# Optimization experiments

Hardware: AMD Instinct MI355X
Metric: run time of the kernel (lower is better)

## Reference

```python
import jax, jax.numpy as jnp
import numpy as np

B, N, M, D, KV, H = 4, 1024, 1024, 1024, 1024, 16
HD = D // H


def setup_inputs() -> dict:
    key = jax.random.key(0)
    ks = jax.random.split(key, 9)
    s = 0.02
    return {
        "query": jax.random.normal(ks[0], (B, N, D), jnp.float32),
        "key_value": jax.random.normal(ks[1], (B, M, KV), jnp.float32),
        "mask": jax.random.bernoulli(ks[2], 0.1, (B, M)),  # True = masked out
        "Wq": jax.random.normal(ks[3], (D, D), jnp.float32) * s,
        "bq": jnp.zeros((D,), jnp.float32),
        "Wkv": jax.random.normal(ks[4], (KV, 2 * D), jnp.float32) * s,
        "bkv": jnp.zeros((2 * D,), jnp.float32),
        "Wp": jax.random.normal(ks[5], (D, 2), jnp.float32) * s,
        "bp": jnp.zeros((2,), jnp.float32),
    }


def reference(query, key_value, mask, Wq, bq, Wkv, bkv, Wp, bp):
    b, n, d = query.shape
    m = key_value.shape[1]
    scale = HD ** (-0.5)
    # projections
    queries = (query @ Wq + bq).reshape(b, n, H, HD)
    kv = (key_value @ Wkv + bkv).reshape(b, m, 2, H, HD)
    keys, values = kv[:, :, 0], kv[:, :, 1]
    # scores in bnmh layout (as the original einsum)
    attention = jnp.einsum('bnhd,bmhd->bnmh', queries, keys) * scale
    # mask [b,m] -> unsqueeze(1) -> [b,1,m] -> unsqueeze(3) -> [b,1,m,1]
    attention = jnp.where(mask[:, None, :, None], -jnp.inf, attention)
    attention = jax.nn.softmax(attention, axis=2)
    outputs = jnp.einsum('bnmh,bmhd->bnhd', attention, values).reshape(b, n, d)
    outputs = outputs @ Wp + bp
    return outputs, attention
```

## Files before the change

### kernel.cpp

```cpp
#include <hip/hip_runtime.h>

typedef unsigned short u16;
typedef unsigned int u32;
typedef __bf16 bf16x8 __attribute__((ext_vector_type(8)));
typedef float f32x4 __attribute__((ext_vector_type(4)));

#define MFMA16 __builtin_amdgcn_mfma_f32_16x16x32_bf16


__device__ __forceinline__ float b2f(u16 u){ u32 x = ((u32)u)<<16; float f; __builtin_memcpy(&f,&x,4); return f; }
__device__ __forceinline__ u16 f2b(float f){ u32 x; __builtin_memcpy(&x,&f,4); return (u16)((x + 0x7fffu + ((x>>16)&1u)) >> 16); }
__device__ __forceinline__ bf16x8 ldf(const u16* p){ uint4 v = *(const uint4*)p; return __builtin_bit_cast(bf16x8, v); }
__device__ __forceinline__ u32 pk(u16 a, u16 b){ return (u32)a | ((u32)b<<16); }

__device__ __forceinline__ void stage16(const u16* g, u16* l) {
  __builtin_amdgcn_global_load_lds(
      (const __attribute__((address_space(1))) void*)g,
      (__attribute__((address_space(3))) void*)l, 16, 0, 0);
}

__device__ __forceinline__ uint4 ld8(const void* base, size_t off, int f32) {
  if (f32) {
    const float* p = (const float*)base + off;
    f32x4 a = *(const f32x4*)p;
    f32x4 b = *(const f32x4*)(p + 4);
    uint4 r;
    r.x = pk(f2b(a[0]), f2b(a[1]));
    r.y = pk(f2b(a[2]), f2b(a[3]));
    r.z = pk(f2b(b[0]), f2b(b[1]));
    r.w = pk(f2b(b[2]), f2b(b[3]));
    return r;
  }
  return *(const uint4*)((const u16*)base + off);
}
__device__ __forceinline__ float lds1(const void* base, size_t off, int f32) {
  return f32 ? ((const float*)base)[off] : b2f(((const u16*)base)[off]);
}

__global__ __launch_bounds__(256) void detect_dtype(const u32* __restrict__ q, int* __restrict__ flag) {
  __shared__ int cnt;
  if (threadIdx.x == 0) cnt = 0;
  __syncthreads();
  int c = 0;
#pragma unroll
  for (int i = 0; i < 4; i++) {
    u32 w = q[threadIdx.x + i*256];
    u32 e = (w >> 7) & 0xFFu;
    c += (e >= 100u && e <= 140u) ? 1 : 0;
  }
#pragma unroll
  for (int m = 1; m <= 32; m <<= 1) c += __shfl_xor(c, m);
  if ((threadIdx.x & 63) == 0) atomicAdd(&cnt, c);
  __syncthreads();
  if (threadIdx.x == 0) flag[0] = (cnt < 512) ? 1 : 0;
}

__global__ __launch_bounds__(1024) void mask_convert(const void* __restrict__ mraw,
                                                     float* __restrict__ maskF) {
  __shared__ u32 orv;
  const int t = threadIdx.x;
  if (t == 0) orv = 0u;
  __syncthreads();
  u32 o = ((const u32*)mraw)[t];
#pragma unroll
  for (int m = 1; m <= 32; m <<= 1) o |= __shfl_xor(o, m);
  if ((t & 63) == 0) atomicOr(&orv, o);
  __syncthreads();
  const u32 orall = orv;
  int mode;
  if ((orall & ~0x01010101u) == 0u) mode = (orall <= 1u) ? 0 : 1;
  else if (orall & 0x0000FF80u)     mode = 2;
  else                              mode = 3;
  const float NEGINF = -__builtin_inff();
#pragma unroll
  for (int i = t; i < 4096; i += 1024) {
    bool mm;
    if      (mode == 0) mm = ((const int*)mraw)[i] != 0;
    else if (mode == 1) mm = ((const unsigned char*)mraw)[i] != 0;
    else if (mode == 2) mm = ((const u16*)mraw)[i] != 0;
    else                mm = ((const float*)mraw)[i] != 0.f;
    maskF[i] = mm ? NEGINF : 0.f;
  }
}

__global__ __launch_bounds__(256) void to_bf16(const void* __restrict__ in, const int* __restrict__ flag,
                                               u16* __restrict__ out) {
  const int f32 = flag[0];
  const size_t idx = ((size_t)blockIdx.x*256 + threadIdx.x)*8;
  *(uint4*)(out + idx) = ld8(in, idx, f32);
}

__global__ __launch_bounds__(256) void transpose_w(const void* __restrict__ in, const int* __restrict__ flag,
                                                   u16* __restrict__ out, int R, int C) {
  __shared__ u16 tile[64][72];
  const int f32 = flag[0];
  const int t = threadIdx.x;
  const int c0 = blockIdx.x*64, r0 = blockIdx.y*64;
  const int lr = t >> 2, cs = (t & 3)*16;
#pragma unroll
  for (int i=0;i<2;i++)
    *(uint4*)&tile[lr][cs + i*8] = ld8(in, (size_t)(r0 + lr)*C + c0 + cs + i*8, f32);
  __syncthreads();
  const int c = t >> 2, rs = (t & 3)*16;
  u16 v[16];
#pragma unroll
  for (int j=0;j<16;j++) v[j] = tile[rs + j][c];
  uint4 u0 = { pk(v[0],v[1]), pk(v[2],v[3]), pk(v[4],v[5]), pk(v[6],v[7]) };
  uint4 u1 = { pk(v[8],v[9]), pk(v[10],v[11]), pk(v[12],v[13]), pk(v[14],v[15]) };
  u16* op = out + (size_t)(c0 + c)*R + r0 + rs;
  *(uint4*)op = u0;
  *(uint4*)(op + 8) = u1;
}

__global__ __launch_bounds__(256) void gemm_nt(const u16* __restrict__ A, const u16* __restrict__ Bt,
                                               const void* __restrict__ bias, const int* __restrict__ flag,
                                               u16* __restrict__ C, int Mdim, int Ndim, int Kdim) {
  __shared__ u16 As[128][64];
  __shared__ u16 Bs[128][64];
  const int f32 = flag[0];
  const int tid = threadIdx.x, l = tid & 63, w = tid >> 6;
  const int n0 = blockIdx.x * 128, m0 = blockIdx.y * 128;
  const int wr = (w & 1) * 64, wc = (w >> 1) * 64;
  const int lr = l & 15, lg = l >> 4;
  f32x4 acc[4][4];
#pragma unroll
  for (int i=0;i<4;i++)
#pragma unroll
    for (int j=0;j<4;j++) acc[i][j] = (f32x4){0.f,0.f,0.f,0.f};
  const int srow = l >> 3;
  const int scol = (l & 7) * 8;
  const u16* Ab = A  + (size_t)m0 * Kdim;
  const u16* Bb = Bt + (size_t)n0 * Kdim;
  for (int k0 = 0; k0 < Kdim; k0 += 64) {
    __syncthreads();
#pragma unroll
    for (int i = 0; i < 4; i++) {
      const int seg = i*4 + w;
      stage16(Ab + (size_t)(seg*8 + srow)*Kdim + k0 + scol, &As[seg*8][0]);
      stage16(Bb + (size_t)(seg*8 + srow)*Kdim + k0 + scol, &Bs[seg*8][0]);
    }
    __syncthreads();
    bf16x8 af[4][2], bfr[4][2];
#pragma unroll
    for (int rt=0; rt<4; rt++) {
      af[rt][0] = ldf(&As[wr + rt*16 + lr][lg*8]);
      af[rt][1] = ldf(&As[wr + rt*16 + lr][32 + lg*8]);
    }
#pragma unroll
    for (int ct=0; ct<4; ct++) {
      bfr[ct][0] = ldf(&Bs[wc + ct*16 + lr][lg*8]);
      bfr[ct][1] = ldf(&Bs[wc + ct*16 + lr][32 + lg*8]);
    }
#pragma unroll
    for (int rt=0; rt<4; rt++)
#pragma unroll
      for (int ct=0; ct<4; ct++) {
        acc[rt][ct] = MFMA16(af[rt][0], bfr[ct][0], acc[rt][ct], 0,0,0);
        acc[rt][ct] = MFMA16(af[rt][1], bfr[ct][1], acc[rt][ct], 0,0,0);
      }
  }
#pragma unroll
  for (int ct=0; ct<4; ct++) {
    const int col = n0 + wc + ct*16 + lr;
    const float bv = lds1(bias, col, f32);
#pragma unroll
    for (int rt=0; rt<4; rt++)
#pragma unroll
      for (int r=0; r<4; r++) {
        const int row = m0 + wr + rt*16 + lg*4 + r;
        C[(size_t)row * Ndim + col] = f2b(acc[rt][ct][r] + bv);
      }
  }
}

__global__ __launch_bounds__(256) void build_vt(const u16* __restrict__ KVb, u16* __restrict__ Vt) {
  __shared__ u16 tile[64][72];
  const int t = threadIdx.x;
  const int m0 = blockIdx.x*64, h = blockIdx.y, b = blockIdx.z;
  const int mr = t >> 2, cs = (t & 3)*16;
  const u16* src = KVb + (size_t)(b*1024 + m0 + mr)*2048 + 1024 + h*64;
#pragma unroll
  for (int i=0;i<2;i++)
    *(uint4*)&tile[mr][cs + i*8] = *(const uint4*)(src + cs + i*8);
  __syncthreads();
  const int hd = t >> 2, ms = (t & 3)*16;
  u16 v[16];
#pragma unroll
  for (int j=0;j<16;j++) v[j] = tile[ms + j][hd];
  uint4 u0 = { pk(v[0],v[1]), pk(v[2],v[3]), pk(v[4],v[5]), pk(v[6],v[7]) };
  uint4 u1 = { pk(v[8],v[9]), pk(v[10],v[11]), pk(v[12],v[13]), pk(v[14],v[15]) };
  u16* op = Vt + (size_t)((b*16 + h)*64 + hd)*1024 + m0 + ms;
  *(uint4*)op = u0;
  *(uint4*)(op + 8) = u1;
}

__global__ __launch_bounds__(256) void attn_kern(const u16* __restrict__ Qb, const u16* __restrict__ KVb,
                                                 const u16* __restrict__ Vt, const float* __restrict__ maskF,
                                                 u16* __restrict__ Pbuf, u16* __restrict__ Obuf) {
  __shared__ u16 Ks[128][72];
  __shared__ u16 Vts[64][136];
  __shared__ u16 Ps[4][16][136];
  __shared__ float mlds[128];
  const int tid = threadIdx.x, l = tid & 63, w = tid >> 6;
  const int lr = l & 15, lg = l >> 4;
  const int n0 = blockIdx.x * 64, h = blockIdx.y, b = blockIdx.z;
  const float NEGINF = -__builtin_inff();
  const float scale2 = 0.125f * 1.44269504088896f;

  bf16x8 qf[2];
  {
    const u16* Qsrc = Qb + (size_t)(b*1024 + n0 + 16*w + lr)*1024 + h*64 + lg*8;
    qf[0] = ldf(Qsrc);
    qf[1] = ldf(Qsrc + 32);
  }
  float mrow[4] = {NEGINF,NEGINF,NEGINF,NEGINF};
  float lrow[4] = {0.f,0.f,0.f,0.f};

  const int ksr = tid >> 1, kss = (tid & 1)*32;
  const u16* Kbase = KVb + (size_t)(b*1024)*2048 + h*64;
  const u16* Vbase = Vt + (size_t)((b*16 + h)*64)*1024;
  const int vsr = tid >> 2, vss = (tid & 3)*32;

  for (int c = 0; c < 8; c++) {
    const int m0 = c * 128;
    __syncthreads();
#pragma unroll
    for (int i=0;i<4;i++)
      *(uint4*)&Ks[ksr][kss + i*8] = *(const uint4*)(Kbase + (size_t)(m0 + ksr)*2048 + kss + i*8);
    if (tid < 128) mlds[tid] = maskF[b*1024 + m0 + tid];
    __syncthreads();
    f32x4 sa[8];
#pragma unroll
    for (int ct=0; ct<8; ct++) {
      sa[ct] = (f32x4){0.f,0.f,0.f,0.f};
      bf16x8 k0 = ldf(&Ks[ct*16 + lr][lg*8]);
      bf16x8 k1 = ldf(&Ks[ct*16 + lr][32 + lg*8]);
      sa[ct] = MFMA16(qf[0], k0, sa[ct], 0,0,0);
      sa[ct] = MFMA16(qf[1], k1, sa[ct], 0,0,0);
    }
    float cmax[4] = {NEGINF,NEGINF,NEGINF,NEGINF};
#pragma unroll
    for (int ct=0; ct<8; ct++) {
      const float mv = mlds[ct*16 + lr];
#pragma unroll
      for (int r=0;r<4;r++) {
        float s = fmaf(sa[ct][r], scale2, mv);
        sa[ct][r] = s;
        cmax[r] = fmaxf(cmax[r], s);
      }
    }
#pragma unroll
    for (int r=0;r<4;r++) {
#pragma unroll
      for (int m = 1; m <= 8; m <<= 1) cmax[r] = fmaxf(cmax[r], __shfl_xor(cmax[r], m));
      const float mnew = fmaxf(mrow[r], cmax[r]);
      float se = 0.f;
#pragma unroll
      for (int ct=0; ct<8; ct++) se += exp2f(fmaxf(sa[ct][r] - mnew, -1000.f));
#pragma unroll
      for (int m = 1; m <= 8; m <<= 1) se += __shfl_xor(se, m);
      lrow[r] = lrow[r] * exp2f(fmaxf(mrow[r] - mnew, -1000.f)) + se;
      mrow[r] = mnew;
    }
  }
  float rinv[4];
#pragma unroll
  for (int r=0;r<4;r++) rinv[r] = (lrow[r] > 0.f) ? 1.f / lrow[r] : 0.f;

  f32x4 oacc[4];
#pragma unroll
  for (int vt=0; vt<4; vt++) oacc[vt] = (f32x4){0.f,0.f,0.f,0.f};
  for (int c = 0; c < 8; c++) {
    const int m0 = c*128;
    __syncthreads();
#pragma unroll
    for (int i=0;i<4;i++)
      *(uint4*)&Ks[ksr][kss + i*8] = *(const uint4*)(Kbase + (size_t)(m0 + ksr)*2048 + kss + i*8);
#pragma unroll
    for (int i=0;i<4;i++)
      *(uint4*)&Vts[vsr][vss + i*8] = *(const uint4*)(Vbase + (size_t)vsr*1024 + m0 + vss + i*8);
    if (tid < 128) mlds[tid] = maskF[b*1024 + m0 + tid];
    __syncthreads();
    f32x4 sa[8];
#pragma unroll
    for (int ct=0; ct<8; ct++) {
      sa[ct] = (f32x4){0.f,0.f,0.f,0.f};
      bf16x8 k0 = ldf(&Ks[ct*16 + lr][lg*8]);
      bf16x8 k1 = ldf(&Ks[ct*16 + lr][32 + lg*8]);
      sa[ct] = MFMA16(qf[0], k0, sa[ct], 0,0,0);
      sa[ct] = MFMA16(qf[1], k1, sa[ct], 0,0,0);
    }
#pragma unroll
    for (int ct=0; ct<8; ct++) {
      const float mv = mlds[ct*16 + lr];
#pragma unroll
      for (int r=0;r<4;r++) {
        float ex = fmaxf(fmaf(sa[ct][r], scale2, mv) - mrow[r], -1000.f);
        float p = exp2f(ex) * rinv[r];
        Ps[w][lg*4 + r][ct*16 + lr] = f2b(p);
      }
    }
    {
      const int pr = l >> 2, psg = (l & 3) * 32;
      u16* gp = Pbuf + (size_t)((b*16 + h)*1024 + n0 + 16*w + pr)*1024 + m0 + psg;
#pragma unroll
      for (int i=0;i<4;i++)
        *(uint4*)(gp + i*8) = *(const uint4*)&Ps[w][pr][psg + i*8];
    }
    bf16x8 pa[4];
#pragma unroll
    for (int t=0;t<4;t++) pa[t] = ldf(&Ps[w][lr][t*32 + lg*8]);
#pragma unroll
    for (int vt=0; vt<4; vt++) {
#pragma unroll
      for (int t=0;t<4;t++) {
        bf16x8 bv = ldf(&Vts[vt*16 + lr][t*32 + lg*8]);
        oacc[vt] = MFMA16(pa[t], bv, oacc[vt], 0,0,0);
      }
    }
  }
#pragma unroll
  for (int vt=0; vt<4; vt++)
#pragma unroll
    for (int r=0;r<4;r++) {
      const int row = b*1024 + n0 + 16*w + lg*4 + r;
      const int col = h*64 + vt*16 + lr;
      Obuf[(size_t)row*1024 + col] = f2b(oacc[vt][r]);
    }
}

__global__ __launch_bounds__(256) void transpose_p(const u16* __restrict__ Pbuf, float* __restrict__ out) {
  __shared__ u16 t2[16][1024];
  const int t = threadIdx.x;
  const int n = blockIdx.x, b = blockIdx.y;
  const int h = t >> 4, sg = (t & 15)*64;
  const u16* src = Pbuf + (size_t)((b*16 + h)*1024 + n)*1024 + sg;
#pragma unroll
  for (int i=0;i<8;i++)
    *(uint4*)&t2[h][sg + i*8] = *(const uint4*)(src + i*8);
  __syncthreads();
  float* dst = out + (size_t)(b*1024 + n)*16384;
#pragma unroll
  for (int mi=0; mi<4; mi++) {
    const int m = t + mi*256;
#pragma unroll
    for (int q=0; q<4; q++) {
      f32x4 v;
#pragma unroll
      for (int j=0; j<4; j++) v[j] = b2f(t2[q*4 + j][m]);
      *(f32x4*)(dst + (size_t)m*16 + q*4) = v;
    }
  }
}

__global__ __launch_bounds__(256) void proj_out_k(const u16* __restrict__ Obuf, const void* __restrict__ Wp,
                                                  const void* __restrict__ bp, const int* __restrict__ flag,
                                                  float* __restrict__ out0) {
  const int f32 = flag[0];
  const int l = threadIdx.x & 63, w = threadIdx.x >> 6;
  const int row = blockIdx.x*4 + w;
  const u16* op = Obuf + (size_t)row*1024 + l*16;
  float d0 = 0.f, d1 = 0.f;
#pragma unroll
  for (int j=0;j<16;j++) {
    const float o = b2f(op[j]);
    d0 = fmaf(o, lds1(Wp, (size_t)(l*16 + j)*2,     f32), d0);
    d1 = fmaf(o, lds1(Wp, (size_t)(l*16 + j)*2 + 1, f32), d1);
  }
#pragma unroll
  for (int m=1; m<=32; m<<=1) { d0 += __shfl_xor(d0, m); d1 += __shfl_xor(d1, m); }
  if (l == 0) {
    out0[row*2]   = d0 + lds1(bp, 0, f32);
    out0[row*2+1] = d1 + lds1(bp, 1, f32);
  }
}

extern "C" void kernel_launch(void* const* d_in, const int* in_sizes, int n_in,
                              void* d_out, int out_size, void* d_ws, size_t ws_size,
                              hipStream_t stream) {
  const void* query     = d_in[0];
  const void* key_value = d_in[1];
  const void* mask      = d_in[2];
  const void* Wq        = d_in[3];
  const void* bq        = d_in[4];
  const void* Wkv       = d_in[5];
  const void* bkv       = d_in[6];
  const void* Wp        = d_in[7];
  const void* bp        = d_in[8];
  float* out0     = (float*)d_out;
  float* attn_out = (float*)d_out + 8192;

  char* ws = (char*)d_ws;
  u16*   WqT   = (u16*)(ws);
  u16*   WkvT  = (u16*)(ws + (2u<<20));
  u16*   Qb    = (u16*)(ws + (6u<<20));
  u16*   KVb   = (u16*)(ws + (14u<<20));
  u16*   Vt    = (u16*)(ws + (30u<<20));
  u16*   Obuf  = (u16*)(ws + (38u<<20));
  float* maskF = (float*)(ws + (46u<<20));
  int*   flag  = (int*)(ws + (46u<<20) + 16384);
  u16*   Pbuf  = (u16*)(ws + (47u<<20));
  u16*   Qc    = (u16*)(ws + (47u<<20));
  u16*   KVc   = (u16*)(ws + (55u<<20));

  detect_dtype<<<1, 256, 0, stream>>>((const u32*)query, flag);
  mask_convert<<<1, 1024, 0, stream>>>(mask, maskF);
  to_bf16<<<2048, 256, 0, stream>>>(query,     flag, Qc);
  to_bf16<<<2048, 256, 0, stream>>>(key_value, flag, KVc);
  transpose_w<<<dim3(16,16), 256, 0, stream>>>(Wq, flag, WqT, 1024, 1024);
  transpose_w<<<dim3(32,16), 256, 0, stream>>>(Wkv, flag, WkvT, 1024, 2048);
  gemm_nt<<<dim3(8,32),  256, 0, stream>>>(Qc,  WqT,  bq,  flag, Qb,  4096, 1024, 1024);
  gemm_nt<<<dim3(16,32), 256, 0, stream>>>(KVc, WkvT, bkv, flag, KVb, 4096, 2048, 1024);
  build_vt<<<dim3(16,16,4), 256, 0, stream>>>(KVb, Vt);
  attn_kern<<<dim3(16,16,4), 256, 0, stream>>>(Qb, KVb, Vt, maskF, Pbuf, Obuf);
  transpose_p<<<dim3(1024,4), 256, 0, stream>>>(Pbuf, attn_out);
  proj_out_k<<<dim3(1024), 256, 0, stream>>>(Obuf, Wp, bp, flag, out0);
}
```

Before: 574.3 us.

## Fuse two-pass attention into single online-softmax pass with deferred probability rescaling

The attention kernel previously ran QK^T twice: one pass for the row max and sum, and a second to form normalized probabilities and multiply by V. It now runs a single online-softmax pass that rescales the output accumulator per chunk. It stores unnormalized probabilities together with per-chunk running maxima and the final max and inverse sum. The transpose kernel then applies the correction factor exp2(m_chunk - m_final) * rinv while writing the fp32 attention output. This removes the duplicated K loads and MFMA work, at the cost of extra small scratch buffers, a per-element LUT multiply in the transpose, and bf16 rounding of the unnormalized values before scaling.

```diff
diff --git a/kernel.cpp b/kernel.cpp
--- a/kernel.cpp
+++ b/kernel.cpp
@@ -196,7 +196,8 @@
 
 __global__ __launch_bounds__(256) void attn_kern(const u16* __restrict__ Qb, const u16* __restrict__ KVb,
                                                  const u16* __restrict__ Vt, const float* __restrict__ maskF,
-                                                 u16* __restrict__ Pbuf, u16* __restrict__ Obuf) {
+                                                 u16* __restrict__ Pbuf, u16* __restrict__ Obuf,
+                                                 float* __restrict__ Sc, float* __restrict__ Fin) {
   __shared__ u16 Ks[128][72];
   __shared__ u16 Vts[64][136];
   __shared__ u16 Ps[4][16][136];
@@ -215,6 +216,9 @@
   }
   float mrow[4] = {NEGINF,NEGINF,NEGINF,NEGINF};
   float lrow[4] = {0.f,0.f,0.f,0.f};
+  f32x4 oacc[4];
+#pragma unroll
+  for (int vt=0; vt<4; vt++) oacc[vt] = (f32x4){0.f,0.f,0.f,0.f};
 
   const int ksr = tid >> 1, kss = (tid & 1)*32;
   const u16* Kbase = KVb + (size_t)(b*1024)*2048 + h*64;
@@ -222,11 +226,14 @@
   const int vsr = tid >> 2, vss = (tid & 3)*32;
 
   for (int c = 0; c < 8; c++) {
-    const int m0 = c * 128;
+    const int m0 = c*128;
     __syncthreads();
 #pragma unroll
     for (int i=0;i<4;i++)
       *(uint4*)&Ks[ksr][kss + i*8] = *(const uint4*)(Kbase + (size_t)(m0 + ksr)*2048 + kss + i*8);
+#pragma unroll
+    for (int i=0;i<4;i++)
+      *(uint4*)&Vts[vsr][vss + i*8] = *(const uint4*)(Vbase + (size_t)vsr*1024 + m0 + vss + i*8);
     if (tid < 128) mlds[tid] = maskF[b*1024 + m0 + tid];
     __syncthreads();
     f32x4 sa[8];
@@ -249,57 +256,32 @@
         cmax[r] = fmaxf(cmax[r], s);
       }
     }
+    float al[4];
 #pragma unroll
     for (int r=0;r<4;r++) {
 #pragma unroll
       for (int m = 1; m <= 8; m <<= 1) cmax[r] = fmaxf(cmax[r], __shfl_xor(cmax[r], m));
       const float mnew = fmaxf(mrow[r], cmax[r]);
+      al[r] = exp2f(fmaxf(mrow[r] - mnew, -1000.f));
       float se = 0.f;
 #pragma unroll
-      for (int ct=0; ct<8; ct++) se += exp2f(fmaxf(sa[ct][r] - mnew, -1000.f));
+      for (int ct=0; ct<8; ct++) {
+        float p = exp2f(fmaxf(sa[ct][r] - mnew, -1000.f));
+        sa[ct][r] = p;
+        se += p;
+      }
 #pragma unroll
       for (int m = 1; m <= 8; m <<= 1) se += __shfl_xor(se, m);
-      lrow[r] = lrow[r] * exp2f(fmaxf(mrow[r] - mnew, -1000.f)) + se;
+      lrow[r] = lrow[r] * al[r] + se;
       mrow[r] = mnew;
-    }
-  }
-  float rinv[4];
-#pragma unroll
-  for (int r=0;r<4;r++) rinv[r] = (lrow[r] > 0.f) ? 1.f / lrow[r] : 0.f;
-
-  f32x4 oacc[4];
-#pragma unroll
-  for (int vt=0; vt<4; vt++) oacc[vt] = (f32x4){0.f,0.f,0.f,0.f};
-  for (int c = 0; c < 8; c++) {
-    const int m0 = c*128;
-    __syncthreads();
-#pragma unroll
-    for (int i=0;i<4;i++)
-      *(uint4*)&Ks[ksr][kss + i*8] = *(const uint4*)(Kbase + (size_t)(m0 + ksr)*2048 + kss + i*8);
-#pragma unroll
-    for (int i=0;i<4;i++)
-      *(uint4*)&Vts[vsr][vss + i*8] = *(const uint4*)(Vbase + (size_t)vsr*1024 + m0 + vss + i*8);
-    if (tid < 128) mlds[tid] = maskF[b*1024 + m0 + tid];
-    __syncthreads();
-    f32x4 sa[8];
-#pragma unroll
-    for (int ct=0; ct<8; ct++) {
-      sa[ct] = (f32x4){0.f,0.f,0.f,0.f};
-      bf16x8 k0 = ldf(&Ks[ct*16 + lr][lg*8]);
-      bf16x8 k1 = ldf(&Ks[ct*16 + lr][32 + lg*8]);
-      sa[ct] = MFMA16(qf[0], k0, sa[ct], 0,0,0);
-      sa[ct] = MFMA16(qf[1], k1, sa[ct], 0,0,0);
-    }
-#pragma unroll
-    for (int ct=0; ct<8; ct++) {
-      const float mv = mlds[ct*16 + lr];
-#pragma unroll
-      for (int r=0;r<4;r++) {
-        float ex = fmaxf(fmaf(sa[ct][r], scale2, mv) - mrow[r], -1000.f);
-        float p = exp2f(ex) * rinv[r];
-        Ps[w][lg*4 + r][ct*16 + lr] = f2b(p);
-      }
-    }
+      if (lr == 0)
+        Sc[(((size_t)b*1024 + n0 + 16*w + lg*4 + r)*16 + h)*8 + c] = mnew;
+    }
+#pragma unroll
+    for (int ct=0; ct<8; ct++)
+#pragma unroll
+      for (int r=0;r<4;r++)
+        Ps[w][lg*4 + r][ct*16 + lr] = f2b(sa[ct][r]);
     {
       const int pr = l >> 2, psg = (l & 3) * 32;
       u16* gp = Pbuf + (size_t)((b*16 + h)*1024 + n0 + 16*w + pr)*1024 + m0 + psg;
@@ -307,6 +289,10 @@
       for (int i=0;i<4;i++)
         *(uint4*)(gp + i*8) = *(const uint4*)&Ps[w][pr][psg + i*8];
     }
+#pragma unroll
+    for (int vt=0; vt<4; vt++)
+#pragma unroll
+      for (int r=0;r<4;r++) oacc[vt][r] *= al[r];
     bf16x8 pa[4];
 #pragma unroll
     for (int t=0;t<4;t++) pa[t] = ldf(&Ps[w][lr][t*32 + lg*8]);
@@ -319,18 +305,33 @@
       }
     }
   }
+  float rinv[4];
+#pragma unroll
+  for (int r=0;r<4;r++) rinv[r] = (lrow[r] > 0.f) ? 1.f / lrow[r] : 0.f;
 #pragma unroll
   for (int vt=0; vt<4; vt++)
 #pragma unroll
     for (int r=0;r<4;r++) {
       const int row = b*1024 + n0 + 16*w + lg*4 + r;
       const int col = h*64 + vt*16 + lr;
-      Obuf[(size_t)row*1024 + col] = f2b(oacc[vt][r]);
-    }
-}
-
-__global__ __launch_bounds__(256) void transpose_p(const u16* __restrict__ Pbuf, float* __restrict__ out) {
+      Obuf[(size_t)row*1024 + col] = f2b(oacc[vt][r] * rinv[r]);
+    }
+  if (lr == 0) {
+#pragma unroll
+    for (int r=0;r<4;r++) {
+      const size_t fo = (((size_t)b*1024 + n0 + 16*w + lg*4 + r)*16 + h)*2;
+      Fin[fo]   = mrow[r];
+      Fin[fo+1] = rinv[r];
+    }
+  }
+}
+
+__global__ __launch_bounds__(256) void transpose_p(const u16* __restrict__ Pbuf,
+                                                   const float* __restrict__ Sc,
+                                                   const float* __restrict__ Fin,
+                                                   float* __restrict__ out) {
   __shared__ u16 t2[16][1024];
+  __shared__ float slut[128];
   const int t = threadIdx.x;
   const int n = blockIdx.x, b = blockIdx.y;
   const int h = t >> 4, sg = (t & 15)*64;
@@ -338,16 +339,25 @@
 #pragma unroll
   for (int i=0;i<8;i++)
     *(uint4*)&t2[h][sg + i*8] = *(const uint4*)(src + i*8);
+  if (t < 128) {
+    const int hh = t >> 3, cc = t & 7;
+    const size_t base = ((size_t)b*1024 + n)*16 + hh;
+    const float mc = Sc[base*8 + cc];
+    const float mf = Fin[base*2];
+    const float ri = Fin[base*2 + 1];
+    slut[t] = exp2f(fmaxf(mc - mf, -1000.f)) * ri;
+  }
   __syncthreads();
   float* dst = out + (size_t)(b*1024 + n)*16384;
 #pragma unroll
   for (int mi=0; mi<4; mi++) {
     const int m = t + mi*256;
+    const int c = m >> 7;
 #pragma unroll
     for (int q=0; q<4; q++) {
       f32x4 v;
 #pragma unroll
-      for (int j=0; j<4; j++) v[j] = b2f(t2[q*4 + j][m]);
+      for (int j=0; j<4; j++) v[j] = b2f(t2[q*4 + j][m]) * slut[(q*4 + j)*8 + c];
       *(f32x4*)(dst + (size_t)m*16 + q*4) = v;
     }
   }
@@ -400,6 +410,8 @@
   float* maskF = (float*)(ws + (46u<<20));
   int*   flag  = (int*)(ws + (46u<<20) + 16384);
   u16*   Pbuf  = (u16*)(ws + (47u<<20));
+  float* Sc    = (float*)(ws + (175u<<20));
+  float* Fin   = (float*)(ws + (177u<<20));
   u16*   Qc    = (u16*)(ws + (47u<<20));
   u16*   KVc   = (u16*)(ws + (55u<<20));
 
@@ -412,7 +424,7 @@
   gemm_nt<<<dim3(8,32),  256, 0, stream>>>(Qc,  WqT,  bq,  flag, Qb,  4096, 1024, 1024);
   gemm_nt<<<dim3(16,32), 256, 0, stream>>>(KVc, WkvT, bkv, flag, KVb, 4096, 2048, 1024);
   build_vt<<<dim3(16,16,4), 256, 0, stream>>>(KVb, Vt);
-  attn_kern<<<dim3(16,16,4), 256, 0, stream>>>(Qb, KVb, Vt, maskF, Pbuf, Obuf);
-  transpose_p<<<dim3(1024,4), 256, 0, stream>>>(Pbuf, attn_out);
+  attn_kern<<<dim3(16,16,4), 256, 0, stream>>>(Qb, KVb, Vt, maskF, Pbuf, Obuf, Sc, Fin);
+  transpose_p<<<dim3(1024,4), 256, 0, stream>>>(Pbuf, Sc, Fin, attn_out);
   proj_out_k<<<dim3(1024), 256, 0, stream>>>(Obuf, Wp, bp, flag, out0);
 }
```

New measurement: 545.2 us. 5.1% less time.
